# Performance work log

Hardware: AMD Instinct MI355X
Metric: run time of the kernel (lower is better)

## Reference

```python
import jax, jax.numpy as jnp
import numpy as np
from jax.ops import segment_sum, segment_min, segment_max

N, E = 25000, 400000
NF, EF = 30, 10
H = 40          # n_hidden (multiple of towers)
T = 5           # towers
F = H           # F_in per tower (divide_input=False)
FO = H // T     # F_out per tower
L = 2           # gnn layers
NC = 2          # classes
EPS_BN = 1e-5


def setup_inputs() -> dict:
    key = jax.random.key(0)
    ks = jax.random.split(key, 24)
    r = lambda k, s, sc=0.1: jax.random.normal(k, s, jnp.float32) * sc
    return {
        "x": jax.random.normal(ks[0], (N, NF), jnp.float32),
        "edge_attr": jax.random.normal(ks[1], (E, EF), jnp.float32),
        "edge_index": jax.random.randint(ks[2], (2, E), 0, N, jnp.int32),
        "node_w": r(ks[3], (NF, H)), "node_b": r(ks[4], (H,)),
        "edge_w": r(ks[5], (EF, H)), "edge_b": r(ks[6], (H,)),
        "enc_w": r(ks[7], (L, H, F)), "enc_b": r(ks[8], (L, F)),
        "pre_w": r(ks[9], (L, T, 3 * F, F)), "pre_b": r(ks[10], (L, T, F)),
        "post_w": r(ks[11], (L, T, 13 * F, FO)), "post_b": r(ks[12], (L, T, FO)),
        "lin_w": r(ks[13], (L, H, H)), "lin_b": r(ks[14], (L, H)),
        "bn_g": jnp.ones((L, H), jnp.float32), "bn_b": jnp.zeros((L, H), jnp.float32),
        "mlp1_w": r(ks[15], (3 * H, 50)), "mlp1_b": r(ks[16], (50,)),
        "mlp2_w": r(ks[17], (50, 25)), "mlp2_b": r(ks[18], (25,)),
        "mlp3_w": r(ks[19], (25, NC)), "mlp3_b": r(ks[20], (NC,)),
    }


def _pna_conv(x, src, dst, e_emb, enc_w, enc_b, pre_w, pre_b, post_w, post_b,
              lin_w, lin_b, cnt, cnt1, amp, att):
    # message: per-tower pre-MLP on cat(x_i=dst, x_j=src, enc(edge_attr))
    e = e_emb @ enc_w + enc_b                                    # [E, F]
    h = jnp.concatenate([x[dst], x[src], e], axis=-1)            # [E, 3F]
    hs = jnp.einsum('ef,tfo->eto', h, pre_w) + pre_b             # [E, T, F]
    # multi-aggregation over incoming edges (index = dst)
    c = cnt1[:, None, None]
    mean = segment_sum(hs, dst, num_segments=N) / c
    msq = segment_sum(hs * hs, dst, num_segments=N) / c
    std = jnp.sqrt(jax.nn.relu(msq - mean * mean) + 1e-5)
    has = (cnt > 0)[:, None, None]
    mn = jnp.where(has, segment_min(hs, dst, num_segments=N), 0.0)
    mx = jnp.where(has, segment_max(hs, dst, num_segments=N), 0.0)
    agg = jnp.concatenate([mean, mn, mx, std], axis=-1)          # [N, T, 4F]
    agg = jnp.concatenate([agg, agg * amp, agg * att], axis=-1)  # [N, T, 12F]
    out = jnp.concatenate(
        [jnp.broadcast_to(x[:, None, :], (N, T, F)), agg], axis=-1)  # [N, T, 13F]
    out = jnp.einsum('ntf,tfo->nto', out, post_w) + post_b       # [N, T, FO]
    return out.reshape(N, T * FO) @ lin_w + lin_b                # [N, H]


def reference(x, edge_attr, node_w, node_b, edge_w, edge_b, enc_w, enc_b,
              pre_w, pre_b, post_w, post_b, lin_w, lin_b, bn_g, bn_b,
              mlp1_w, mlp1_b, mlp2_w, mlp2_b, mlp3_w, mlp3_b, edge_index):
    src, dst = edge_index[0], edge_index[1]
    cnt = segment_sum(jnp.ones((E,), jnp.float32), dst, num_segments=N)  # in-degree
    cnt1 = jnp.maximum(cnt, 1.0)                                 # deg.clamp_(1)
    log_deg = jnp.log(cnt1 + 1.0)
    avg_log = jnp.mean(jnp.log(cnt + 1.0))                       # PNA avg_deg['log']
    amp = (log_deg / avg_log)[:, None, None]
    att = (avg_log / log_deg)[:, None, None]
    h = x @ node_w + node_b                                      # node embedding
    e_emb = edge_attr @ edge_w + edge_b                          # edge embedding
    for i in range(L):
        c = _pna_conv(h, src, dst, e_emb, enc_w[i], enc_b[i], pre_w[i], pre_b[i],
                      post_w[i], post_b[i], lin_w[i], lin_b[i], cnt, cnt1, amp, att)
        mu = jnp.mean(c, axis=0)
        var = jnp.mean((c - mu) ** 2, axis=0)                    # BatchNorm (batch stats)
        cbn = (c - mu) / jnp.sqrt(var + EPS_BN) * bn_g[i] + bn_b[i]
        h = (h + jax.nn.relu(cbn)) / 2.0
    z = jax.nn.relu(jnp.concatenate([h[src], h[dst]], axis=-1))  # [E, 2H]
    z = jnp.concatenate([z, e_emb], axis=-1)                     # [E, 3H]
    z = jax.nn.relu(z @ mlp1_w + mlp1_b)
    z = jax.nn.relu(z @ mlp2_w + mlp2_b)
    return z @ mlp3_w + mlp3_b                                   # [E, NC]
```

## Files before the change

kernel.cpp:

```cpp
#include <hip/hip_runtime.h>
#include <hip/hip_bf16.h>
#include <cstdint>
#include <cstddef>

#define NN 25000
#define NE 400000
#define NFD 30
#define EFD 10
#define H 40
#define T 5
#define FO 8
#define LAYERS 2
#define TF 200
#define BASE_W 800
#define PSTR 52
#define WS_PAD 532
#define REC 12
#define WCN 416
#define WCK 64
#define SHP 72
#define EPSV 1e-5f

typedef __attribute__((ext_vector_type(8))) short bf16x8;
typedef __attribute__((ext_vector_type(4))) float f32x4;

__device__ inline short bfbits(float v) {
    __hip_bfloat16 b = __float2bfloat16(v);
    return *(short*)&b;
}

__global__ __launch_bounds__(256) void k_deg(const int* __restrict__ dst, int* __restrict__ cnt) {
    int e = blockIdx.x * 256 + threadIdx.x;
    if (e < NE) atomicAdd(&cnt[dst[e]], 1);
}

__global__ __launch_bounds__(256) void k_avglog(const int* __restrict__ cnt, float* __restrict__ slot) {
    __shared__ float red[256];
    float s = 0.0f;
    for (int i = blockIdx.x * 256 + threadIdx.x; i < NN; i += gridDim.x * 256)
        s += logf((float)cnt[i] + 1.0f);
    red[threadIdx.x] = s; __syncthreads();
    for (int o = 128; o > 0; o >>= 1) {
        if (threadIdx.x < o) red[threadIdx.x] += red[threadIdx.x + o];
        __syncthreads();
    }
    if (threadIdx.x == 0) atomicAdd(slot, red[0]);
}

__global__ __launch_bounds__(256) void k_node(const float* __restrict__ x, const float* __restrict__ w,
                                              const float* __restrict__ b, float* __restrict__ h,
                                              const int* __restrict__ cnt, const float* __restrict__ slot,
                                              float* __restrict__ amp, float* __restrict__ att) {
    int id = blockIdx.x * 256 + threadIdx.x;
    if (id < NN) {
        float avg = slot[0] / (float)NN;
        float c1 = fmaxf((float)cnt[id], 1.0f);
        float lg = logf(c1 + 1.0f);
        amp[id] = lg / avg;
        att[id] = avg / lg;
    }
    if (id >= NN * H) return;
    int n = id / H, j = id - n * H;
    const float* xr = x + (size_t)n * NFD;
    float acc = b[j];
    #pragma unroll
    for (int m = 0; m < NFD; m++) acc += xr[m] * w[m * H + j];
    h[id] = acc;
}

__global__ __launch_bounds__(1024) void k_scan(const int* __restrict__ cnt, int* __restrict__ offs) {
    __shared__ int wsum[16];
    int tid = threadIdx.x;
    int lane = tid & 63, wv = tid >> 6;
    int runbase = 0;
    for (int base = 0; base < NN; base += 4096) {
        int i0 = base + tid * 4;
        int4 v = make_int4(0, 0, 0, 0);
        if (i0 < NN) v = *(const int4*)(cnt + i0);
        int tsum = v.x + v.y + v.z + v.w;
        int x = tsum;
        #pragma unroll
        for (int o = 1; o < 64; o <<= 1) {
            int y = __shfl_up(x, o);
            if (lane >= o) x += y;
        }
        if (lane == 63) wsum[wv] = x;
        __syncthreads();
        if (wv == 0 && lane < 16) {
            int wsv = wsum[lane];
            #pragma unroll
            for (int o = 1; o < 16; o <<= 1) {
                int y = __shfl_up(wsv, o);
                if (lane >= o) wsv += y;
            }
            wsum[lane] = wsv;
        }
        __syncthreads();
        int wpref = (wv > 0) ? wsum[wv - 1] : 0;
        int excl = runbase + wpref + x - tsum;
        if (i0 < NN) {
            offs[i0]     = excl;
            offs[i0 + 1] = excl + v.x;
            offs[i0 + 2] = excl + v.x + v.y;
            offs[i0 + 3] = excl + v.x + v.y + v.z;
        }
        runbase += wsum[15];
        __syncthreads();
    }
    if (tid == 0) offs[NN] = runbase;
}

__global__ __launch_bounds__(256) void k_scatter(const int* __restrict__ src, const int* __restrict__ dst,
                                                 const float* __restrict__ edge_attr,
                                                 const int* __restrict__ offs, int* __restrict__ fill,
                                                 float* __restrict__ ea_csr, int* __restrict__ pdst) {
    int e = blockIdx.x * 256 + threadIdx.x;
    if (e >= NE) return;
    int d = dst[e];
    int p = offs[d] + atomicAdd(&fill[d], 1);
    const float2* ear = (const float2*)(edge_attr + (size_t)e * EFD);
    float2 v0 = ear[0], v1 = ear[1], v2 = ear[2], v3 = ear[3], v4 = ear[4];
    float4* o = (float4*)(ea_csr + (size_t)p * REC);
    o[0] = make_float4(v0.x, v0.y, v1.x, v1.y);
    o[1] = make_float4(v2.x, v2.y, v3.x, v3.y);
    o[2] = make_float4(v4.x, v4.y, __int_as_float(src[e]), __int_as_float(e));
    pdst[p] = d;
}

__global__ __launch_bounds__(256) void k_prep1(const float* __restrict__ enc_w, const float* __restrict__ enc_b,
                                               const float* __restrict__ edge_w, const float* __restrict__ edge_b,
                                               const float* __restrict__ pre_w, const float* __restrict__ pre_b,
                                               const float* __restrict__ w1, const float* __restrict__ b1,
                                               float* __restrict__ W3e, float* __restrict__ dvecF,
                                               __hip_bfloat16* __restrict__ Wcat,
                                               float* __restrict__ W1e, float* __restrict__ b1e, int layer) {
    int id = blockIdx.x * 256 + threadIdx.x;
    if (id < EFD * TF) {
        int m = id / TF, j = id - m * TF;
        int t = j / H, f = j - t * H;
        const float* ew = enc_w + (size_t)layer * H * H;
        const float* pw = pre_w + (size_t)(layer * T + t) * 120 * H;
        float acc = 0.0f;
        for (int k = 0; k < H; k++) {
            float wk = edge_w[m * H + k];
            float g = 0.0f;
            #pragma unroll
            for (int o = 0; o < H; o++) g += ew[k * H + o] * pw[(80 + o) * H + f];
            acc += wk * g;
        }
        W3e[m * TF + j] = acc;
        if (m == 0) {
            const float* eb = enc_b + (size_t)layer * H;
            float dacc = pre_b[(size_t)(layer * T + t) * H + f];
            for (int o = 0; o < H; o++) {
                float ebe = eb[o];
                #pragma unroll
                for (int k = 0; k < H; k++) ebe += edge_b[k] * ew[k * H + o];
                dacc += ebe * pw[(80 + o) * H + f];
            }
            dvecF[j] = dacc;
        }
    } else if (id < EFD * TF + WCN * WCK) {
        int id2 = id - EFD * TF;
        int j = id2 / WCK, k = id2 - j * WCK;
        float val = 0.0f;
        if (k < H) {
            if (j < TF) {
                int t = j / H, f = j - t * H;
                val = pre_w[((size_t)(layer * T + t) * 120 + k) * H + f];
            } else if (j >= 208 && j < 208 + TF) {
                int j2 = j - 208;
                int t = j2 / H, f = j2 - t * H;
                val = pre_w[((size_t)(layer * T + t) * 120 + H + k) * H + f];
            }
        }
        Wcat[id2] = __float2bfloat16(val);
    } else if (layer == 0 && id < EFD * TF + WCN * WCK + EFD * 50) {
        int id2 = id - EFD * TF - WCN * WCK;
        int m = id2 / 50, o = id2 - m * 50;
        float acc = 0.0f;
        #pragma unroll
        for (int k = 0; k < H; k++) acc += edge_w[m * H + k] * w1[(80 + k) * 50 + o];
        W1e[m * 50 + o] = acc;
        if (m == 0) {
            float bacc = b1[o];
            #pragma unroll
            for (int k = 0; k < H; k++) bacc += edge_b[k] * w1[(80 + k) * 50 + o];
            b1e[o] = bacc;
        }
    }
}

__global__ __launch_bounds__(256) void k_abm(float* h, const float* __restrict__ cbuf,
                                             const float* __restrict__ bnsum, const float* __restrict__ bnsq,
                                             const float* __restrict__ bng, const float* __restrict__ bnb,
                                             int doBN,
                                             const __hip_bfloat16* __restrict__ Wcat,
                                             float* __restrict__ A, __hip_bfloat16* __restrict__ Bbf) {
    __shared__ short sh[64 * SHP];
    int tid = threadIdx.x;
    int n0 = blockIdx.x * 64;
    int nodes = NN - n0; if (nodes > 64) nodes = 64;
    for (int i = tid; i < 64 * SHP; i += 256) sh[i] = 0;
    __syncthreads();
    float invN = 1.0f / (float)NN;
    for (int i = tid; i < nodes * H; i += 256) {
        int f = i % H;
        float hv = h[(size_t)n0 * H + i];
        float hn;
        if (doBN) {
            float mu = bnsum[f] * invN;
            float var = bnsq[f] * invN - mu * mu;
            float c = (cbuf[(size_t)n0 * H + i] - mu) * rsqrtf(var + EPSV) * bng[f] + bnb[f];
            hn = (hv + fmaxf(c, 0.0f)) * 0.5f;
            h[(size_t)n0 * H + i] = hn;
        } else {
            hn = hv;
        }
        sh[(i / H) * SHP + f] = bfbits(hn);
    }
    __syncthreads();

    int wv = tid >> 6, lane = tid & 63;
    int q = lane >> 4, c16 = lane & 15;
    const short* arow = sh + (wv * 16 + c16) * SHP + q * 8;
    bf16x8 a0 = *(const bf16x8*)(arow);
    bf16x8 a1 = *(const bf16x8*)(arow + 32);
    int gm = n0 + wv * 16 + q * 4;

    for (int jt = 0; jt < 26; jt++) {
        int col = jt * 16 + c16;
        const short* wrow = (const short*)Wcat + (size_t)col * WCK + q * 8;
        bf16x8 b0 = *(const bf16x8*)(wrow);
        bf16x8 b1 = *(const bf16x8*)(wrow + 32);
        f32x4 acc = {0.0f, 0.0f, 0.0f, 0.0f};
        acc = __builtin_amdgcn_mfma_f32_16x16x32_bf16(a0, b0, acc, 0, 0, 0);
        acc = __builtin_amdgcn_mfma_f32_16x16x32_bf16(a1, b1, acc, 0, 0, 0);
        if (col < TF) {
            #pragma unroll
            for (int r = 0; r < 4; r++) {
                int row = gm + r;
                if (row < NN) A[(size_t)row * TF + col] = acc[r];
            }
        } else if (col >= 208) {
            int c2 = col - 208;
            if (c2 < TF) {
                #pragma unroll
                for (int r = 0; r < 4; r++) {
                    int row = gm + r;
                    if (row < NN) Bbf[(size_t)row * TF + c2] = __float2bfloat16(acc[r]);
                }
            }
        }
    }
}

__global__ __launch_bounds__(256) void k_agg(const float* __restrict__ ea_csr,
                                             const __hip_bfloat16* __restrict__ Bbf,
                                             const float* __restrict__ A, const float* __restrict__ w3e,
                                             const float* __restrict__ dvecF, const int* __restrict__ cnt,
                                             const int* __restrict__ offs, float* __restrict__ base) {
    int tid = threadIdx.x;
    int lane = tid & 63;
    int n = __builtin_amdgcn_readfirstlane((int)(blockIdx.x * 4 + (tid >> 6)));
    int deg = cnt[n];
    int start = offs[n];
    bool comp = lane < TF / 4;
    float4 w3q[EFD];
    float4 dj4 = make_float4(0, 0, 0, 0), a4 = make_float4(0, 0, 0, 0);
    if (comp) {
        #pragma unroll
        for (int m = 0; m < EFD; m++) w3q[m] = *(const float4*)(w3e + m * TF + 4 * lane);
        dj4 = *(const float4*)(dvecF + 4 * lane);
        a4  = *(const float4*)(A + (size_t)n * TF + 4 * lane);
    }
    float sx = 0, sy = 0, sz = 0, sw_ = 0;
    float qx = 0, qy = 0, qz = 0, qw = 0;
    float mnx = 3.4e38f, mny = 3.4e38f, mnz = 3.4e38f, mnw = 3.4e38f;
    float mxx = -3.4e38f, mxy = -3.4e38f, mxz = -3.4e38f, mxw = -3.4e38f;
    const float4* recb = (const float4*)ea_csr + (size_t)start * 3;
    const uint16_t* Bu = (const uint16_t*)Bbf;

    auto edge = [&](float4 qa, float4 qb, float4 qc, uint2 bv) {
        float b0 = __uint_as_float(bv.x << 16);
        float b1 = __uint_as_float(bv.x & 0xffff0000u);
        float b2 = __uint_as_float(bv.y << 16);
        float b3 = __uint_as_float(bv.y & 0xffff0000u);
        float eav[EFD] = {qa.x, qa.y, qa.z, qa.w, qb.x, qb.y, qb.z, qb.w, qc.x, qc.y};
        float cx = dj4.x, cy = dj4.y, cz = dj4.z, cw = dj4.w;
        #pragma unroll
        for (int m = 0; m < EFD; m++) {
            cx = fmaf(eav[m], w3q[m].x, cx);
            cy = fmaf(eav[m], w3q[m].y, cy);
            cz = fmaf(eav[m], w3q[m].z, cz);
            cw = fmaf(eav[m], w3q[m].w, cw);
        }
        float ux = b0 + cx, uy = b1 + cy, uz = b2 + cz, uw = b3 + cw;
        sx += ux; qx = fmaf(ux, ux, qx); mnx = fminf(mnx, ux); mxx = fmaxf(mxx, ux);
        sy += uy; qy = fmaf(uy, uy, qy); mny = fminf(mny, uy); mxy = fmaxf(mxy, uy);
        sz += uz; qz = fmaf(uz, uz, qz); mnz = fminf(mnz, uz); mxz = fmaxf(mxz, uz);
        sw_ += uw; qw = fmaf(uw, uw, qw); mnw = fminf(mnw, uw); mxw = fmaxf(mxw, uw);
    };

    int r = 0;
    for (; r + 4 <= deg; r += 4) {
        float4 qa0 = recb[(r + 0) * 3], qb0 = recb[(r + 0) * 3 + 1], qc0 = recb[(r + 0) * 3 + 2];
        float4 qa1 = recb[(r + 1) * 3], qb1 = recb[(r + 1) * 3 + 1], qc1 = recb[(r + 1) * 3 + 2];
        float4 qa2 = recb[(r + 2) * 3], qb2 = recb[(r + 2) * 3 + 1], qc2 = recb[(r + 2) * 3 + 2];
        float4 qa3 = recb[(r + 3) * 3], qb3 = recb[(r + 3) * 3 + 1], qc3 = recb[(r + 3) * 3 + 2];
        int s0 = __float_as_int(qc0.z), s1 = __float_as_int(qc1.z);
        int s2 = __float_as_int(qc2.z), s3 = __float_as_int(qc3.z);
        if (comp) {
            uint2 v0 = *(const uint2*)(Bu + (size_t)s0 * TF + 4 * lane);
            uint2 v1 = *(const uint2*)(Bu + (size_t)s1 * TF + 4 * lane);
            uint2 v2 = *(const uint2*)(Bu + (size_t)s2 * TF + 4 * lane);
            uint2 v3 = *(const uint2*)(Bu + (size_t)s3 * TF + 4 * lane);
            edge(qa0, qb0, qc0, v0);
            edge(qa1, qb1, qc1, v1);
            edge(qa2, qb2, qc2, v2);
            edge(qa3, qb3, qc3, v3);
        }
    }
    for (; r < deg; r++) {
        float4 qa = recb[r * 3], qb = recb[r * 3 + 1], qc = recb[r * 3 + 2];
        int sn = __float_as_int(qc.z);
        if (comp) {
            uint2 bv = *(const uint2*)(Bu + (size_t)sn * TF + 4 * lane);
            edge(qa, qb, qc, bv);
        }
    }
    if (comp) {
        float d = (float)deg, c1 = fmaxf(d, 1.0f);
        float inv = 1.0f / c1;
        float mex = (d * a4.x + sx) * inv, mey = (d * a4.y + sy) * inv;
        float mez = (d * a4.z + sz) * inv, mew = (d * a4.w + sw_) * inv;
        float msx = (d * a4.x * a4.x + 2.0f * a4.x * sx + qx) * inv;
        float msy = (d * a4.y * a4.y + 2.0f * a4.y * sy + qy) * inv;
        float msz = (d * a4.z * a4.z + 2.0f * a4.z * sz + qz) * inv;
        float msw = (d * a4.w * a4.w + 2.0f * a4.w * sw_ + qw) * inv;
        float4 mean4 = make_float4(mex, mey, mez, mew);
        float4 sd4 = make_float4(sqrtf(fmaxf(msx - mex * mex, 0.0f) + EPSV),
                                 sqrtf(fmaxf(msy - mey * mey, 0.0f) + EPSV),
                                 sqrtf(fmaxf(msz - mez * mez, 0.0f) + EPSV),
                                 sqrtf(fmaxf(msw - mew * mew, 0.0f) + EPSV));
        bool has = deg > 0;
        float4 mnv4 = has ? make_float4(a4.x + mnx, a4.y + mny, a4.z + mnz, a4.w + mnw)
                          : make_float4(0, 0, 0, 0);
        float4 mxv4 = has ? make_float4(a4.x + mxx, a4.y + mxy, a4.z + mxz, a4.w + mxw)
                          : make_float4(0, 0, 0, 0);
        int j0 = 4 * lane;
        int t = j0 / H, f = j0 - t * H;
        float* bb = base + (size_t)n * BASE_W + t * 160 + f;
        *(float4*)(bb)       = mean4;
        *(float4*)(bb + 40)  = mnv4;
        *(float4*)(bb + 80)  = mxv4;
        *(float4*)(bb + 120) = sd4;
    }
}

__global__ __launch_bounds__(256) void k_post(const float* __restrict__ h, const float* __restrict__ base,
                                              const float* __restrict__ amp, const float* __restrict__ att,
                                              const float* __restrict__ post_w, const float* __restrict__ post_b,
                                              float* __restrict__ cpre, int layer) {
    __shared__ float ws[FO * WS_PAD];
    int tid = threadIdx.x;
    int t = blockIdx.y;
    const float* pwsrc = post_w + (size_t)(layer * T + t) * 520 * FO;
    for (int i = tid; i < 520 * FO; i += 256) {
        int g = i >> 3, o = i & 7;
        ws[o * WS_PAD + g] = pwsrc[i];
    }
    __syncthreads();
    int slot = tid >> 3, o = tid & 7;
    int n0 = blockIdx.x * 64 + slot * 2;
    if (n0 >= NN) return;
    int n1 = n0 + 1;
    bool two = (n1 < NN);
    if (!two) n1 = n0;
    const float* wrow = ws + o * WS_PAD;
    float am0 = amp[n0], at0 = att[n0];
    float am1 = amp[n1], at1 = att[n1];
    float pb = post_b[(size_t)(layer * T + t) * FO + o];
    float acc0 = pb, acc1 = pb;
    const float4* hx0 = (const float4*)(h + (size_t)n0 * H);
    const float4* hx1 = (const float4*)(h + (size_t)n1 * H);
    #pragma unroll
    for (int g4 = 0; g4 < 10; g4++) {
        float4 wv = *(const float4*)(wrow + g4 * 4);
        float4 x0 = hx0[g4], x1 = hx1[g4];
        acc0 += x0.x * wv.x + x0.y * wv.y + x0.z * wv.z + x0.w * wv.w;
        acc1 += x1.x * wv.x + x1.y * wv.y + x1.z * wv.z + x1.w * wv.w;
    }
    const float4* b0 = (const float4*)(base + (size_t)n0 * BASE_W + t * 160);
    const float4* b1 = (const float4*)(base + (size_t)n1 * BASE_W + t * 160);
    #pragma unroll 8
    for (int g4 = 0; g4 < 40; g4++) {
        float4 wa = *(const float4*)(wrow + 40 + g4 * 4);
        float4 wb = *(const float4*)(wrow + 200 + g4 * 4);
        float4 wc = *(const float4*)(wrow + 360 + g4 * 4);
        float4 v0 = b0[g4], v1 = b1[g4];
        acc0 += v0.x * (wa.x + am0 * wb.x + at0 * wc.x)
              + v0.y * (wa.y + am0 * wb.y + at0 * wc.y)
              + v0.z * (wa.z + am0 * wb.z + at0 * wc.z)
              + v0.w * (wa.w + am0 * wb.w + at0 * wc.w);
        acc1 += v1.x * (wa.x + am1 * wb.x + at1 * wc.x)
              + v1.y * (wa.y + am1 * wb.y + at1 * wc.y)
              + v1.z * (wa.z + am1 * wb.z + at1 * wc.z)
              + v1.w * (wa.w + am1 * wb.w + at1 * wc.w);
    }
    cpre[(size_t)n0 * H + t * FO + o] = acc0;
    if (two) cpre[(size_t)n1 * H + t * FO + o] = acc1;
}

__global__ __launch_bounds__(256) void k_linbn(const float* __restrict__ cpre, const float* __restrict__ lin_w,
                                               const float* __restrict__ lin_b, float* __restrict__ cbuf,
                                               float* __restrict__ bnsum, float* __restrict__ bnsq, int layer) {
    __shared__ float scp[240];
    __shared__ float red[80];
    int tid = threadIdx.x;
    int j = tid % H, nl = tid / H;
    const float* lw = lin_w + (size_t)layer * H * H;
    float wcol[H];
    #pragma unroll
    for (int k = 0; k < H; k++) wcol[k] = lw[k * H + j];
    float lb = lin_b[(size_t)layer * H + j];
    float lsum = 0.0f, lsq = 0.0f;
    for (int n0 = blockIdx.x * 6; n0 < NN; n0 += gridDim.x * 6) {
        int nn = NN - n0; if (nn > 6) nn = 6;
        if (tid < nn * H) scp[tid] = cpre[(size_t)n0 * H + tid];
        __syncthreads();
        if (nl < nn) {
            float acc = lb;
            #pragma unroll
            for (int k = 0; k < H; k++) acc += scp[nl * H + k] * wcol[k];
            cbuf[(size_t)(n0 + nl) * H + j] = acc;
            lsum += acc; lsq += acc * acc;
        }
        __syncthreads();
    }
    if (tid < 80) red[tid] = 0.0f;
    __syncthreads();
    if (nl < 6) { atomicAdd(&red[j], lsum); atomicAdd(&red[40 + j], lsq); }
    __syncthreads();
    if (tid < 40) atomicAdd(&bnsum[tid], red[tid]);
    else if (tid < 80) atomicAdd(&bnsq[tid - 40], red[tid]);
}

__global__ __launch_bounds__(256) void k_prep2(const float* __restrict__ h, const float* __restrict__ cbuf,
                                               const float* __restrict__ bnsum, const float* __restrict__ bnsq,
                                               const float* __restrict__ bng, const float* __restrict__ bnb,
                                               const float* __restrict__ w1,
                                               float* __restrict__ P1, float* __restrict__ P2) {
    __shared__ float sh[5 * H];
    int tid = threadIdx.x;
    int n0 = blockIdx.x * 5;
    if (tid < 5 * H) {
        int j = tid % H;
        float invN = 1.0f / (float)NN;
        float mu = bnsum[j] * invN;
        float var = bnsq[j] * invN - mu * mu;
        float inv = rsqrtf(var + EPSV);
        float cv = (cbuf[(size_t)n0 * H + tid] - mu) * inv * bng[j] + bnb[j];
        sh[tid] = (h[(size_t)n0 * H + tid] + fmaxf(cv, 0.0f)) * 0.5f;
    }
    __syncthreads();
    if (tid >= 250) return;
    int nl = tid / 50, o = tid - nl * 50;
    const float* hr = sh + nl * H;
    float a1 = 0.0f, a2 = 0.0f;
    #pragma unroll
    for (int f = 0; f < H; f++) {
        float v = fmaxf(hr[f], 0.0f);
        a1 += v * w1[f * 50 + o];
        a2 += v * w1[(H + f) * 50 + o];
    }
    P1[(size_t)(n0 + nl) * PSTR + o] = a1;
    P2[(size_t)(n0 + nl) * PSTR + o] = a2;
}

__global__ __launch_bounds__(256) void k_mlp(const float* __restrict__ ea_csr, const int* __restrict__ pdst,
                                             const float* __restrict__ P1, const float* __restrict__ P2,
                                             const float* __restrict__ W1e, const float* __restrict__ b1e,
                                             const float* __restrict__ w2, const float* __restrict__ b2,
                                             const float* __restrict__ w3, const float* __restrict__ b3,
                                             float* __restrict__ out) {
    int p = blockIdx.x * 256 + threadIdx.x;
    if (p >= NE) return;
    const float4* rec = (const float4*)ea_csr + (size_t)p * 3;
    float4 r0 = rec[0], r1 = rec[1], r2 = rec[2];
    int s = __float_as_int(r2.z), eid = __float_as_int(r2.w);
    int d = pdst[p];
    float ea[EFD] = {r0.x, r0.y, r0.z, r0.w, r1.x, r1.y, r1.z, r1.w, r2.x, r2.y};

    float z1[52];
    const float4* p1r = (const float4*)(P1 + (size_t)s * PSTR);
    const float4* p2r = (const float4*)(P2 + (size_t)d * PSTR);
    #pragma unroll
    for (int i = 0; i < 13; i++) {
        float4 a = p1r[i], b = p2r[i];
        z1[4 * i]     = a.x + b.x;
        z1[4 * i + 1] = a.y + b.y;
        z1[4 * i + 2] = a.z + b.z;
        z1[4 * i + 3] = a.w + b.w;
    }
    #pragma unroll
    for (int k = 0; k < 50; k++) z1[k] += b1e[k];
    #pragma unroll
    for (int m = 0; m < EFD; m++) {
        float v = ea[m];
        #pragma unroll
        for (int k = 0; k < 50; k++) z1[k] = fmaf(v, W1e[m * 50 + k], z1[k]);
    }
    float z2[25];
    #pragma unroll
    for (int o = 0; o < 25; o++) z2[o] = b2[o];
    #pragma unroll
    for (int k = 0; k < 50; k++) {
        float v = fmaxf(z1[k], 0.0f);
        #pragma unroll
        for (int o = 0; o < 25; o++) z2[o] = fmaf(v, w2[k * 25 + o], z2[o]);
    }
    float o0 = b3[0], o1 = b3[1];
    #pragma unroll
    for (int k = 0; k < 25; k++) {
        float v = fmaxf(z2[k], 0.0f);
        o0 = fmaf(v, w3[k * 2], o0);
        o1 = fmaf(v, w3[k * 2 + 1], o1);
    }
    *(float2*)(out + (size_t)eid * 2) = make_float2(o0, o1);
}

extern "C" void kernel_launch(void* const* d_in, const int* in_sizes, int n_in,
                              void* d_out, int out_size, void* d_ws, size_t ws_size,
                              hipStream_t stream) {
    const float* x         = (const float*)d_in[0];
    const float* edge_attr = (const float*)d_in[1];
    const int*   eidx      = (const int*)  d_in[2];
    const float* node_w    = (const float*)d_in[3];
    const float* node_b    = (const float*)d_in[4];
    const float* edge_w    = (const float*)d_in[5];
    const float* edge_b    = (const float*)d_in[6];
    const float* enc_w     = (const float*)d_in[7];
    const float* enc_b     = (const float*)d_in[8];
    const float* pre_w     = (const float*)d_in[9];
    const float* pre_b     = (const float*)d_in[10];
    const float* post_w    = (const float*)d_in[11];
    const float* post_b    = (const float*)d_in[12];
    const float* lin_w     = (const float*)d_in[13];
    const float* lin_b     = (const float*)d_in[14];
    const float* bn_g      = (const float*)d_in[15];
    const float* bn_b      = (const float*)d_in[16];
    const float* w1 = (const float*)d_in[17];
    const float* b1 = (const float*)d_in[18];
    const float* w2 = (const float*)d_in[19];
    const float* b2 = (const float*)d_in[20];
    const float* w3 = (const float*)d_in[21];
    const float* b3 = (const float*)d_in[22];
    const int* srcp = eidx;
    const int* dstp = eidx + NE;
    float* out = (float*)d_out;

    char* ws = (char*)d_ws;
    size_t off = 0;
    auto alloc = [&](size_t bytes) -> char* {
        char* p = ws + off;
        off += (bytes + 255) & ~(size_t)255;
        return p;
    };
    float* h      = (float*)alloc((size_t)NN * H * 4);
    float* Abuf   = (float*)alloc((size_t)NN * TF * 4);
    float* cbuf   = (float*)alloc((size_t)NN * H * 4);
    __hip_bfloat16* Bbf = (__hip_bfloat16*)alloc((size_t)NN * TF * 2 + 256);
    float* base   = (float*)alloc((size_t)NN * BASE_W * 4);
    float* cpre   = (float*)alloc((size_t)NN * H * 4);
    float* ea_csr = (float*)alloc((size_t)NE * REC * 4);
    int* pdst     = (int*)alloc((size_t)NE * 4);
    float* W3e    = (float*)alloc((size_t)EFD * TF * 4);
    float* dvecF  = (float*)alloc((size_t)TF * 4);
    __hip_bfloat16* Wcat = (__hip_bfloat16*)alloc((size_t)WCN * WCK * 2);
    float* P1     = (float*)alloc((size_t)NN * PSTR * 4);
    float* P2     = (float*)alloc((size_t)NN * PSTR * 4);
    float* W1e    = (float*)alloc((size_t)EFD * 50 * 4);
    float* b1e    = (float*)alloc((size_t)64 * 4);
    float* amp    = (float*)alloc((size_t)NN * 4);
    float* att    = (float*)alloc((size_t)NN * 4);
    int* offs     = (int*)alloc((size_t)(NN + 1) * 4);
    size_t zoff = off;
    int* cnt_i    = (int*)alloc((size_t)NN * 4);
    int* fill     = (int*)alloc((size_t)NN * 4);
    float* avgs   = (float*)alloc(256);
    float* bnz    = (float*)alloc(1024);
    size_t zsize = off - zoff;
    if (off > ws_size) return;

    hipMemsetAsync(cnt_i, 0, zsize, stream);

    k_deg<<<(NE + 255) / 256, 256, 0, stream>>>(dstp, cnt_i);
    k_avglog<<<64, 256, 0, stream>>>(cnt_i, avgs);
    k_node<<<(NN * H + 255) / 256, 256, 0, stream>>>(x, node_w, node_b, h, cnt_i, avgs, amp, att);
    k_scan<<<1, 1024, 0, stream>>>(cnt_i, offs);
    k_scatter<<<(NE + 255) / 256, 256, 0, stream>>>(srcp, dstp, edge_attr, offs, fill, ea_csr, pdst);

    int prep1_grid = (EFD * TF + WCN * WCK + EFD * 50 + 255) / 256;
    for (int layer = 0; layer < LAYERS; layer++) {
        float* bnzL = bnz + layer * 128;
        k_prep1<<<prep1_grid, 256, 0, stream>>>(
            enc_w, enc_b, edge_w, edge_b, pre_w, pre_b, w1, b1,
            W3e, dvecF, Wcat, W1e, b1e, layer);
        float* bnzP = bnz + (layer - 1) * 128;
        k_abm<<<(NN + 63) / 64, 256, 0, stream>>>(
            h, cbuf, (layer > 0) ? bnzP : bnz, (layer > 0) ? bnzP + 40 : bnz,
            bn_g + (size_t)(layer > 0 ? layer - 1 : 0) * H,
            bn_b + (size_t)(layer > 0 ? layer - 1 : 0) * H,
            (layer > 0) ? 1 : 0, Wcat, Abuf, Bbf);
        k_agg<<<NN / 4, 256, 0, stream>>>(ea_csr, Bbf, Abuf, W3e, dvecF, cnt_i, offs, base);
        k_post<<<dim3((NN + 63) / 64, T), 256, 0, stream>>>(h, base, amp, att, post_w, post_b, cpre, layer);
        k_linbn<<<1024, 256, 0, stream>>>(cpre, lin_w, lin_b, cbuf, bnzL, bnzL + 40, layer);
    }
    k_prep2<<<NN / 5, 256, 0, stream>>>(h, cbuf, bnz + 128, bnz + 168,
                                        bn_g + H, bn_b + H, w1, P1, P2);
    k_mlp<<<(NE + 255) / 256, 256, 0, stream>>>(ea_csr, pdst, P1, P2, W1e, b1e, w2, b2, w3, b3, out);
}
```

Baseline: 595.0 us.

## Compute PNA post-MLP with bf16 MFMA using prepacked post weights

```diff
diff --git a/kernel.cpp b/kernel.cpp
--- a/kernel.cpp
+++ b/kernel.cpp
@@ -14,11 +14,13 @@
 #define TF 200
 #define BASE_W 800
 #define PSTR 52
-#define WS_PAD 532
 #define REC 12
 #define WCN 416
 #define WCK 64
 #define SHP 72
+#define WPK 224
+#define WPROWS 160
+#define SDP 33
 #define EPSV 1e-5f
 
 typedef __attribute__((ext_vector_type(8))) short bf16x8;
@@ -130,9 +132,11 @@
 __global__ __launch_bounds__(256) void k_prep1(const float* __restrict__ enc_w, const float* __restrict__ enc_b,
                                                const float* __restrict__ edge_w, const float* __restrict__ edge_b,
                                                const float* __restrict__ pre_w, const float* __restrict__ pre_b,
+                                               const float* __restrict__ post_w,
                                                const float* __restrict__ w1, const float* __restrict__ b1,
                                                float* __restrict__ W3e, float* __restrict__ dvecF,
                                                __hip_bfloat16* __restrict__ Wcat,
+                                               __hip_bfloat16* __restrict__ Wpost,
                                                float* __restrict__ W1e, float* __restrict__ b1e, int layer) {
     int id = blockIdx.x * 256 + threadIdx.x;
     if (id < EFD * TF) {
@@ -175,8 +179,22 @@
             }
         }
         Wcat[id2] = __float2bfloat16(val);
-    } else if (layer == 0 && id < EFD * TF + WCN * WCK + EFD * 50) {
-        int id2 = id - EFD * TF - WCN * WCK;
+    } else if (id < EFD * TF + WCN * WCK + WPROWS * WPK) {
+        int id3 = id - EFD * TF - WCN * WCK;
+        int row = id3 / WPK, k = id3 - row * WPK;
+        int t = row >> 5, rt = row & 31;
+        int tile = rt >> 4, col = rt & 15, o = col & 7;
+        int g = -1;
+        if (k < 160) {
+            if (tile == 0) g = (col < 8) ? (40 + k) : (200 + k);
+            else if (col < 8) g = 360 + k;
+        } else if (k < 200 && tile == 0 && col < 8) {
+            g = k - 160;
+        }
+        float val = (g >= 0) ? post_w[(((size_t)(layer * T + t)) * 520 + g) * FO + o] : 0.0f;
+        Wpost[id3] = __float2bfloat16(val);
+    } else if (layer == 0 && id < EFD * TF + WCN * WCK + WPROWS * WPK + EFD * 50) {
+        int id2 = id - EFD * TF - WCN * WCK - WPROWS * WPK;
         int m = id2 / 50, o = id2 - m * 50;
         float acc = 0.0f;
         #pragma unroll
@@ -358,58 +376,72 @@
     }
 }
 
-__global__ __launch_bounds__(256) void k_post(const float* __restrict__ h, const float* __restrict__ base,
-                                              const float* __restrict__ amp, const float* __restrict__ att,
-                                              const float* __restrict__ post_w, const float* __restrict__ post_b,
-                                              float* __restrict__ cpre, int layer) {
-    __shared__ float ws[FO * WS_PAD];
+__global__ __launch_bounds__(256) void k_postm(const float* __restrict__ h, const float* __restrict__ base,
+                                               const float* __restrict__ amp, const float* __restrict__ att,
+                                               const __hip_bfloat16* __restrict__ Wpost,
+                                               const float* __restrict__ post_b,
+                                               float* __restrict__ cpre, int layer) {
+    __shared__ short sh[64 * WPK];
+    __shared__ float sD[4][16 * SDP];
     int tid = threadIdx.x;
-    int t = blockIdx.y;
-    const float* pwsrc = post_w + (size_t)(layer * T + t) * 520 * FO;
-    for (int i = tid; i < 520 * FO; i += 256) {
-        int g = i >> 3, o = i & 7;
-        ws[o * WS_PAD + g] = pwsrc[i];
-    }
-    __syncthreads();
-    int slot = tid >> 3, o = tid & 7;
-    int n0 = blockIdx.x * 64 + slot * 2;
-    if (n0 >= NN) return;
-    int n1 = n0 + 1;
-    bool two = (n1 < NN);
-    if (!two) n1 = n0;
-    const float* wrow = ws + o * WS_PAD;
-    float am0 = amp[n0], at0 = att[n0];
-    float am1 = amp[n1], at1 = att[n1];
-    float pb = post_b[(size_t)(layer * T + t) * FO + o];
-    float acc0 = pb, acc1 = pb;
-    const float4* hx0 = (const float4*)(h + (size_t)n0 * H);
-    const float4* hx1 = (const float4*)(h + (size_t)n1 * H);
-    #pragma unroll
-    for (int g4 = 0; g4 < 10; g4++) {
-        float4 wv = *(const float4*)(wrow + g4 * 4);
-        float4 x0 = hx0[g4], x1 = hx1[g4];
-        acc0 += x0.x * wv.x + x0.y * wv.y + x0.z * wv.z + x0.w * wv.w;
-        acc1 += x1.x * wv.x + x1.y * wv.y + x1.z * wv.z + x1.w * wv.w;
-    }
-    const float4* b0 = (const float4*)(base + (size_t)n0 * BASE_W + t * 160);
-    const float4* b1 = (const float4*)(base + (size_t)n1 * BASE_W + t * 160);
-    #pragma unroll 8
-    for (int g4 = 0; g4 < 40; g4++) {
-        float4 wa = *(const float4*)(wrow + 40 + g4 * 4);
-        float4 wb = *(const float4*)(wrow + 200 + g4 * 4);
-        float4 wc = *(const float4*)(wrow + 360 + g4 * 4);
-        float4 v0 = b0[g4], v1 = b1[g4];
-        acc0 += v0.x * (wa.x + am0 * wb.x + at0 * wc.x)
-              + v0.y * (wa.y + am0 * wb.y + at0 * wc.y)
-              + v0.z * (wa.z + am0 * wb.z + at0 * wc.z)
-              + v0.w * (wa.w + am0 * wb.w + at0 * wc.w);
-        acc1 += v1.x * (wa.x + am1 * wb.x + at1 * wc.x)
-              + v1.y * (wa.y + am1 * wb.y + at1 * wc.y)
-              + v1.z * (wa.z + am1 * wb.z + at1 * wc.z)
-              + v1.w * (wa.w + am1 * wb.w + at1 * wc.w);
-    }
-    cpre[(size_t)n0 * H + t * FO + o] = acc0;
-    if (two) cpre[(size_t)n1 * H + t * FO + o] = acc1;
+    int n0 = blockIdx.x * 64;
+    for (int i = tid; i < 64 * 10; i += 256) {
+        int node = i / 10, k4 = i - node * 10;
+        int gn = n0 + node;
+        float4 v = (gn < NN) ? *(const float4*)(h + (size_t)gn * H + k4 * 4)
+                             : make_float4(0, 0, 0, 0);
+        short4 s4 = make_short4(bfbits(v.x), bfbits(v.y), bfbits(v.z), bfbits(v.w));
+        *(short4*)(sh + node * WPK + 160 + k4 * 4) = s4;
+    }
+    for (int i = tid; i < 64 * 6; i += 256) {
+        int node = i / 6, k4 = i - node * 6;
+        *(short4*)(sh + node * WPK + 200 + k4 * 4) = make_short4(0, 0, 0, 0);
+    }
+    int wv = tid >> 6, lane = tid & 63;
+    int q = lane >> 4, c16 = lane & 15;
+    const short* arow = sh + (wv * 16 + c16) * WPK + q * 8;
+    float* sd = sD[wv];
+
+    for (int t = 0; t < T; t++) {
+        for (int i = tid; i < 64 * 40; i += 256) {
+            int node = i / 40, k4 = i - node * 40;
+            int gn = n0 + node;
+            float4 v = (gn < NN) ? *(const float4*)(base + (size_t)gn * BASE_W + t * 160 + k4 * 4)
+                                 : make_float4(0, 0, 0, 0);
+            short4 s4 = make_short4(bfbits(v.x), bfbits(v.y), bfbits(v.z), bfbits(v.w));
+            *(short4*)(sh + node * WPK + k4 * 4) = s4;
+        }
+        __syncthreads();
+        const short* wb0 = (const short*)Wpost + ((size_t)t * 32 + c16) * WPK + q * 8;
+        const short* wb1 = (const short*)Wpost + ((size_t)t * 32 + 16 + c16) * WPK + q * 8;
+        f32x4 acc0 = {0, 0, 0, 0}, acc1 = {0, 0, 0, 0};
+        #pragma unroll
+        for (int c = 0; c < 7; c++) {
+            bf16x8 av = *(const bf16x8*)(arow + c * 32);
+            bf16x8 b0 = *(const bf16x8*)(wb0 + c * 32);
+            bf16x8 b1 = *(const bf16x8*)(wb1 + c * 32);
+            acc0 = __builtin_amdgcn_mfma_f32_16x16x32_bf16(av, b0, acc0, 0, 0, 0);
+            acc1 = __builtin_amdgcn_mfma_f32_16x16x32_bf16(av, b1, acc1, 0, 0, 0);
+        }
+        #pragma unroll
+        for (int r = 0; r < 4; r++) {
+            sd[(q * 4 + r) * SDP + c16] = acc0[r];
+            sd[(q * 4 + r) * SDP + 16 + c16] = acc1[r];
+        }
+        #pragma unroll
+        for (int kk = 0; kk < 2; kk++) {
+            int idx = kk * 64 + lane;
+            int m = idx >> 3, oo = idx & 7;
+            int gn = n0 + wv * 16 + m;
+            if (gn < NN) {
+                float am = amp[gn], at = att[gn];
+                float val = sd[m * SDP + oo] + am * sd[m * SDP + 8 + oo] + at * sd[m * SDP + 16 + oo]
+                          + post_b[((size_t)(layer * T + t)) * FO + oo];
+                cpre[(size_t)gn * H + t * FO + oo] = val;
+            }
+        }
+        __syncthreads();
+    }
 }
 
 __global__ __launch_bounds__(256) void k_linbn(const float* __restrict__ cpre, const float* __restrict__ lin_w,
@@ -577,7 +609,8 @@
     int* pdst     = (int*)alloc((size_t)NE * 4);
     float* W3e    = (float*)alloc((size_t)EFD * TF * 4);
     float* dvecF  = (float*)alloc((size_t)TF * 4);
-    __hip_bfloat16* Wcat = (__hip_bfloat16*)alloc((size_t)WCN * WCK * 2);
+    __hip_bfloat16* Wcat  = (__hip_bfloat16*)alloc((size_t)WCN * WCK * 2);
+    __hip_bfloat16* Wpost = (__hip_bfloat16*)alloc((size_t)WPROWS * WPK * 2);
     float* P1     = (float*)alloc((size_t)NN * PSTR * 4);
     float* P2     = (float*)alloc((size_t)NN * PSTR * 4);
     float* W1e    = (float*)alloc((size_t)EFD * 50 * 4);
@@ -601,12 +634,13 @@
     k_scan<<<1, 1024, 0, stream>>>(cnt_i, offs);
     k_scatter<<<(NE + 255) / 256, 256, 0, stream>>>(srcp, dstp, edge_attr, offs, fill, ea_csr, pdst);
 
-    int prep1_grid = (EFD * TF + WCN * WCK + EFD * 50 + 255) / 256;
+    int prep1_items = EFD * TF + WCN * WCK + WPROWS * WPK + EFD * 50;
+    int prep1_grid = (prep1_items + 255) / 256;
     for (int layer = 0; layer < LAYERS; layer++) {
         float* bnzL = bnz + layer * 128;
         k_prep1<<<prep1_grid, 256, 0, stream>>>(
-            enc_w, enc_b, edge_w, edge_b, pre_w, pre_b, w1, b1,
-            W3e, dvecF, Wcat, W1e, b1e, layer);
+            enc_w, enc_b, edge_w, edge_b, pre_w, pre_b, post_w, w1, b1,
+            W3e, dvecF, Wcat, Wpost, W1e, b1e, layer);
         float* bnzP = bnz + (layer - 1) * 128;
         k_abm<<<(NN + 63) / 64, 256, 0, stream>>>(
             h, cbuf, (layer > 0) ? bnzP : bnz, (layer > 0) ? bnzP + 40 : bnz,
@@ -614,7 +648,7 @@
             bn_b + (size_t)(layer > 0 ? layer - 1 : 0) * H,
             (layer > 0) ? 1 : 0, Wcat, Abuf, Bbf);
         k_agg<<<NN / 4, 256, 0, stream>>>(ea_csr, Bbf, Abuf, W3e, dvecF, cnt_i, offs, base);
-        k_post<<<dim3((NN + 63) / 64, T), 256, 0, stream>>>(h, base, amp, att, post_w, post_b, cpre, layer);
+        k_postm<<<(NN + 63) / 64, 256, 0, stream>>>(h, base, amp, att, Wpost, post_b, cpre, layer);
         k_linbn<<<1024, 256, 0, stream>>>(cpre, lin_w, lin_b, cbuf, bnzL, bnzL + 40, layer);
     }
     k_prep2<<<NN / 5, 256, 0, stream>>>(h, cbuf, bnz + 128, bnz + 168,
```

Result: no change. 601.3 us (+1.1%).

## Process aggregation nodes in descending-degree order via counting-sort permutation

Applied to the files above, without the earlier changes.

```diff
diff --git a/kernel.cpp b/kernel.cpp
--- a/kernel.cpp
+++ b/kernel.cpp
@@ -19,6 +19,7 @@
 #define WCN 416
 #define WCK 64
 #define SHP 72
+#define DB 2048
 #define EPSV 1e-5f
 
 typedef __attribute__((ext_vector_type(8))) short bf16x8;
@@ -50,14 +51,17 @@
 __global__ __launch_bounds__(256) void k_node(const float* __restrict__ x, const float* __restrict__ w,
                                               const float* __restrict__ b, float* __restrict__ h,
                                               const int* __restrict__ cnt, const float* __restrict__ slot,
-                                              float* __restrict__ amp, float* __restrict__ att) {
+                                              float* __restrict__ amp, float* __restrict__ att,
+                                              int* __restrict__ dhist) {
     int id = blockIdx.x * 256 + threadIdx.x;
     if (id < NN) {
         float avg = slot[0] / (float)NN;
-        float c1 = fmaxf((float)cnt[id], 1.0f);
+        int dg = cnt[id];
+        float c1 = fmaxf((float)dg, 1.0f);
         float lg = logf(c1 + 1.0f);
         amp[id] = lg / avg;
         att[id] = avg / lg;
+        atomicAdd(&dhist[dg < DB ? dg : DB - 1], 1);
     }
     if (id >= NN * H) return;
     int n = id / H, j = id - n * H;
@@ -108,6 +112,48 @@
         __syncthreads();
     }
     if (tid == 0) offs[NN] = runbase;
+}
+
+__global__ __launch_bounds__(1024) void k_dscan(const int* __restrict__ dhist, int* __restrict__ doff) {
+    __shared__ int wsum[16];
+    int tid = threadIdx.x;
+    int lane = tid & 63, wv = tid >> 6;
+    int bA = DB - 1 - 2 * tid;
+    int bB = bA - 1;
+    int cA = dhist[bA], cB = (bB >= 0) ? dhist[bB] : 0;
+    int tsum = cA + cB;
+    int x = tsum;
+    #pragma unroll
+    for (int o = 1; o < 64; o <<= 1) {
+        int y = __shfl_up(x, o);
+        if (lane >= o) x += y;
+    }
+    if (lane == 63) wsum[wv] = x;
+    __syncthreads();
+    if (wv == 0 && lane < 16) {
+        int wsv = wsum[lane];
+        #pragma unroll
+        for (int o = 1; o < 16; o <<= 1) {
+            int y = __shfl_up(wsv, o);
+            if (lane >= o) wsv += y;
+        }
+        wsum[lane] = wsv;
+    }
+    __syncthreads();
+    int wpref = (wv > 0) ? wsum[wv - 1] : 0;
+    int excl = wpref + x - tsum;
+    doff[bA] = excl;
+    if (bB >= 0) doff[bB] = excl + cA;
+}
+
+__global__ __launch_bounds__(256) void k_dscatter(const int* __restrict__ cnt, const int* __restrict__ doff,
+                                                  int* __restrict__ dfill, int* __restrict__ perm) {
+    int n = blockIdx.x * 256 + threadIdx.x;
+    if (n >= NN) return;
+    int dg = cnt[n];
+    int b = dg < DB ? dg : DB - 1;
+    int pos = doff[b] + atomicAdd(&dfill[b], 1);
+    perm[pos] = n;
 }
 
 __global__ __launch_bounds__(256) void k_scatter(const int* __restrict__ src, const int* __restrict__ dst,
@@ -259,10 +305,12 @@
                                              const __hip_bfloat16* __restrict__ Bbf,
                                              const float* __restrict__ A, const float* __restrict__ w3e,
                                              const float* __restrict__ dvecF, const int* __restrict__ cnt,
-                                             const int* __restrict__ offs, float* __restrict__ base) {
+                                             const int* __restrict__ offs, const int* __restrict__ perm,
+                                             float* __restrict__ base) {
     int tid = threadIdx.x;
     int lane = tid & 63;
-    int n = __builtin_amdgcn_readfirstlane((int)(blockIdx.x * 4 + (tid >> 6)));
+    int pidx = blockIdx.x * 4 + (tid >> 6);
+    int n = __builtin_amdgcn_readfirstlane(perm[pidx]);
     int deg = cnt[n];
     int start = offs[n];
     bool comp = lane < TF / 4;
@@ -585,11 +633,15 @@
     float* amp    = (float*)alloc((size_t)NN * 4);
     float* att    = (float*)alloc((size_t)NN * 4);
     int* offs     = (int*)alloc((size_t)(NN + 1) * 4);
+    int* doff     = (int*)alloc((size_t)DB * 4);
+    int* perm     = (int*)alloc((size_t)NN * 4);
     size_t zoff = off;
     int* cnt_i    = (int*)alloc((size_t)NN * 4);
     int* fill     = (int*)alloc((size_t)NN * 4);
     float* avgs   = (float*)alloc(256);
     float* bnz    = (float*)alloc(1024);
+    int* dhist    = (int*)alloc((size_t)DB * 4);
+    int* dfill    = (int*)alloc((size_t)DB * 4);
     size_t zsize = off - zoff;
     if (off > ws_size) return;
 
@@ -597,9 +649,11 @@
 
     k_deg<<<(NE + 255) / 256, 256, 0, stream>>>(dstp, cnt_i);
     k_avglog<<<64, 256, 0, stream>>>(cnt_i, avgs);
-    k_node<<<(NN * H + 255) / 256, 256, 0, stream>>>(x, node_w, node_b, h, cnt_i, avgs, amp, att);
+    k_node<<<(NN * H + 255) / 256, 256, 0, stream>>>(x, node_w, node_b, h, cnt_i, avgs, amp, att, dhist);
     k_scan<<<1, 1024, 0, stream>>>(cnt_i, offs);
     k_scatter<<<(NE + 255) / 256, 256, 0, stream>>>(srcp, dstp, edge_attr, offs, fill, ea_csr, pdst);
+    k_dscan<<<1, 1024, 0, stream>>>(dhist, doff);
+    k_dscatter<<<(NN + 255) / 256, 256, 0, stream>>>(cnt_i, doff, dfill, perm);
 
     int prep1_grid = (EFD * TF + WCN * WCK + EFD * 50 + 255) / 256;
     for (int layer = 0; layer < LAYERS; layer++) {
@@ -613,7 +667,7 @@
             bn_g + (size_t)(layer > 0 ? layer - 1 : 0) * H,
             bn_b + (size_t)(layer > 0 ? layer - 1 : 0) * H,
             (layer > 0) ? 1 : 0, Wcat, Abuf, Bbf);
-        k_agg<<<NN / 4, 256, 0, stream>>>(ea_csr, Bbf, Abuf, W3e, dvecF, cnt_i, offs, base);
+        k_agg<<<NN / 4, 256, 0, stream>>>(ea_csr, Bbf, Abuf, W3e, dvecF, cnt_i, offs, perm, base);
         k_post<<<dim3((NN + 63) / 64, T), 256, 0, stream>>>(h, base, amp, att, post_w, post_b, cpre, layer);
         k_linbn<<<1024, 256, 0, stream>>>(cpre, lin_w, lin_b, cbuf, bnzL, bnzL + 40, layer);
     }
```

After: 713.6 us. 19.9% more time.
